# Kernel optimization log

Measured on AMD Instinct MI355X. Metric: run time of the kernel, lower is better.

## Reference

```python
import jax, jax.numpy as jnp
import numpy as np

H = 128

def setup_inputs() -> dict:
    key = jax.random.key(0)
    ks = jax.random.split(key, 7)
    x = jax.random.normal(ks[0], (4, 65536, H), dtype=jnp.float32)
    # Linear(3H -> H) and Linear(H -> H), torch-style fan-in init scale
    W1 = jax.random.normal(ks[1], (3 * H, H), dtype=jnp.float32) / np.sqrt(3 * H)
    b1 = jax.random.normal(ks[2], (H,), dtype=jnp.float32) * 0.01
    W2 = jax.random.normal(ks[3], (H, H), dtype=jnp.float32) / np.sqrt(H)
    b2 = jax.random.normal(ks[4], (H,), dtype=jnp.float32) * 0.01
    gamma = jnp.ones((H,), dtype=jnp.float32)
    beta = jnp.zeros((H,), dtype=jnp.float32)
    return {"x": x, "W1": W1, "b1": b1, "W2": W2, "b2": b2, "gamma": gamma, "beta": beta}


def _layernorm(h, gamma, beta, eps=1e-5):
    mu = jnp.mean(h, axis=-1, keepdims=True)
    var = jnp.var(h, axis=-1, keepdims=True)
    return (h - mu) * jax.lax.rsqrt(var + eps) * gamma + beta


def reference(x, W1, b1, W2, b2, gamma, beta):
    # circular neighbor gather along node dim
    prev_x = jnp.roll(x, 1, axis=1)
    next_x = jnp.roll(x, -1, axis=1)
    cat = jnp.concatenate([prev_x, x, next_x], axis=-1)  # [B, N, 3H]
    h = jax.nn.relu(jnp.einsum('bnc,ch->bnh', cat, W1) + b1)
    delta = jnp.einsum('bnh,hk->bnk', h, W2) + b2
    return jax.nn.relu(_layernorm(x + delta, gamma, beta))
```

## Files before the change

### kernel.cpp

```cpp
#include <hip/hip_runtime.h>


typedef __bf16 bf16x8 __attribute__((ext_vector_type(8)));
typedef __bf16 bf16x4 __attribute__((ext_vector_type(4)));
typedef float  f32x4  __attribute__((ext_vector_type(4)));

#define H      128
#define NB     65536
#define TILE   64
#define XS     136
#define HSS    136
#define PSS    18
#define NTILES 4096
#define GRID   512

__global__ __launch_bounds__(256, 2)
void cbb_kernel(const float* __restrict__ x, const float* __restrict__ W1,
                const float* __restrict__ b1, const float* __restrict__ W2,
                const float* __restrict__ b2, const float* __restrict__ gamma,
                const float* __restrict__ beta, float* __restrict__ out) {
    __shared__ __align__(16) char raw[(66 * XS + 64 * HSS) * 2];
    __bf16* xs = (__bf16*)raw;
    __bf16* hs = xs + 66 * XS;
    __shared__ __align__(16) __bf16 w2s[16384];
    __shared__ __align__(16) float2 ps2[64 * PSS];

    const int tid  = threadIdx.x;
    const int wid  = tid >> 6;
    const int lane = tid & 63;
    const int l    = lane & 15;
    const int g    = lane >> 4;
    const int col0 = wid * 32;

    const f32x4 b1v[2] = { *(const f32x4*)(b1 + col0 + g * 4),
                           *(const f32x4*)(b1 + col0 + 16 + g * 4) };
    const f32x4 b2v[2] = { *(const f32x4*)(b2 + col0 + g * 4),
                           *(const f32x4*)(b2 + col0 + 16 + g * 4) };
    const f32x4 gmv[2] = { *(const f32x4*)(gamma + col0 + g * 4),
                           *(const f32x4*)(gamma + col0 + 16 + g * 4) };
    const f32x4 btv[2] = { *(const f32x4*)(beta + col0 + g * 4),
                           *(const f32x4*)(beta + col0 + 16 + g * 4) };

    bf16x8 w1f[12][2];
#pragma unroll
    for (int ks = 0; ks < 12; ++ks) {
#pragma unroll
        for (int ct = 0; ct < 2; ++ct) {
            const int cc = col0 + ct * 16 + l;
            bf16x8 f;
#pragma unroll
            for (int j = 0; j < 8; ++j)
                f[j] = (__bf16)W1[(ks * 32 + g * 8 + j) * H + cc];
            w1f[ks][ct] = f;
        }
    }

    for (int idx = tid; idx < 16384; idx += 256) {
        const int j  = idx & 7;
        const int ln = (idx >> 3) & 63;
        const int ct = (idx >> 9) & 1;
        const int ks = (idx >> 10) & 3;
        const int w  = idx >> 12;
        const int row = ks * 32 + (ln >> 4) * 8 + j;
        const int col = w * 32 + ct * 16 + (ln & 15);
        w2s[idx] = (__bf16)W2[row * H + col];
    }
    const __bf16* w2w = w2s + wid * 4096;

    float4 xreg[8];
    float4 xhalo;
    {
        const int t  = blockIdx.x;
        const int b  = t >> 10;
        const int n0 = (t & 1023) << 6;
        const size_t rowbase = (size_t)b * NB;
#pragma unroll
        for (int s = 0; s < 8; ++s) {
            const int q = tid + s * 256;
            const int r = q >> 5, c = q & 31;
            const int grow = (n0 - 1 + r + NB) & (NB - 1);
            xreg[s] = *(const float4*)(x + ((rowbase + grow) * H + c * 4));
        }
        if (tid < 64) {
            const int q = 2048 + tid;
            const int r = q >> 5, c = q & 31;
            const int grow = (n0 - 1 + r + NB) & (NB - 1);
            xhalo = *(const float4*)(x + ((rowbase + grow) * H + c * 4));
        }
    }

    for (int t = blockIdx.x; t < NTILES; t += GRID) {
        const int b  = t >> 10;
        const int n0 = (t & 1023) << 6;
        const size_t rowbase = (size_t)b * NB;

        __syncthreads();

#pragma unroll
        for (int s = 0; s < 8; ++s) {
            const int q = tid + s * 256;
            const int r = q >> 5, c = q & 31;
            bf16x4 v4;
            v4[0] = (__bf16)xreg[s].x; v4[1] = (__bf16)xreg[s].y;
            v4[2] = (__bf16)xreg[s].z; v4[3] = (__bf16)xreg[s].w;
            *(bf16x4*)(xs + r * XS + c * 4) = v4;
        }
        if (tid < 64) {
            const int q = 2048 + tid;
            const int r = q >> 5, c = q & 31;
            bf16x4 v4;
            v4[0] = (__bf16)xhalo.x; v4[1] = (__bf16)xhalo.y;
            v4[2] = (__bf16)xhalo.z; v4[3] = (__bf16)xhalo.w;
            *(bf16x4*)(xs + r * XS + c * 4) = v4;
        }
        __syncthreads();

        if (t + GRID < NTILES) {
            const int tn  = t + GRID;
            const int bn  = tn >> 10;
            const int n0n = (tn & 1023) << 6;
            const size_t rbn = (size_t)bn * NB;
#pragma unroll
            for (int s = 0; s < 8; ++s) {
                const int q = tid + s * 256;
                const int r = q >> 5, c = q & 31;
                const int grow = (n0n - 1 + r + NB) & (NB - 1);
                xreg[s] = *(const float4*)(x + ((rbn + grow) * H + c * 4));
            }
            if (tid < 64) {
                const int q = 2048 + tid;
                const int r = q >> 5, c = q & 31;
                const int grow = (n0n - 1 + r + NB) & (NB - 1);
                xhalo = *(const float4*)(x + ((rbn + grow) * H + c * 4));
            }
        }

        f32x4 acc[4][2];
#pragma unroll
        for (int rt = 0; rt < 4; ++rt)
#pragma unroll
            for (int ct = 0; ct < 2; ++ct)
                acc[rt][ct] = (f32x4){0.f, 0.f, 0.f, 0.f};

        __builtin_amdgcn_s_setprio(1);
#pragma unroll
        for (int ks = 0; ks < 12; ++ks) {
            const int k  = ks * 32 + g * 8;
            const int ro = k >> 7, kc = k & 127;
#pragma unroll
            for (int rt = 0; rt < 4; ++rt) {
                const bf16x8 a = *(const bf16x8*)(xs + (rt * 16 + l + ro) * XS + kc);
                acc[rt][0] = __builtin_amdgcn_mfma_f32_16x16x32_bf16(w1f[ks][0], a, acc[rt][0], 0, 0, 0);
                acc[rt][1] = __builtin_amdgcn_mfma_f32_16x16x32_bf16(w1f[ks][1], a, acc[rt][1], 0, 0, 0);
            }
        }
        __builtin_amdgcn_s_setprio(0);

#pragma unroll
        for (int rt = 0; rt < 4; ++rt) {
#pragma unroll
            for (int ct = 0; ct < 2; ++ct) {
                bf16x4 hv;
#pragma unroll
                for (int i = 0; i < 4; ++i)
                    hv[i] = (__bf16)fmaxf(acc[rt][ct][i] + b1v[ct][i], 0.f);
                *(bf16x4*)(hs + (rt * 16 + l) * HSS + col0 + ct * 16 + g * 4) = hv;
            }
        }
        __syncthreads();

        f32x4 acc2[4][2];
#pragma unroll
        for (int rt = 0; rt < 4; ++rt)
#pragma unroll
            for (int ct = 0; ct < 2; ++ct)
                acc2[rt][ct] = (f32x4){0.f, 0.f, 0.f, 0.f};

        __builtin_amdgcn_s_setprio(1);
#pragma unroll
        for (int ks = 0; ks < 4; ++ks) {
            const bf16x8 wf0 = *(const bf16x8*)(w2w + ks * 1024 + lane * 8);
            const bf16x8 wf1 = *(const bf16x8*)(w2w + ks * 1024 + 512 + lane * 8);
#pragma unroll
            for (int rt = 0; rt < 4; ++rt) {
                const bf16x8 a = *(const bf16x8*)(hs + (rt * 16 + l) * HSS + ks * 32 + g * 8);
                acc2[rt][0] = __builtin_amdgcn_mfma_f32_16x16x32_bf16(wf0, a, acc2[rt][0], 0, 0, 0);
                acc2[rt][1] = __builtin_amdgcn_mfma_f32_16x16x32_bf16(wf1, a, acc2[rt][1], 0, 0, 0);
            }
        }
        __builtin_amdgcn_s_setprio(0);

#pragma unroll
        for (int rt = 0; rt < 4; ++rt) {
#pragma unroll
            for (int ct = 0; ct < 2; ++ct) {
                const bf16x4 xv = *(const bf16x4*)(xs + (rt * 16 + l + 1) * XS + col0 + ct * 16 + g * 4);
#pragma unroll
                for (int i = 0; i < 4; ++i)
                    acc2[rt][ct][i] += b2v[ct][i] + (float)xv[i];
            }
        }

#pragma unroll
        for (int rt = 0; rt < 4; ++rt) {
            float s = 0.f, qq = 0.f;
#pragma unroll
            for (int ct = 0; ct < 2; ++ct)
#pragma unroll
                for (int i = 0; i < 4; ++i) {
                    const float v = acc2[rt][ct][i];
                    s += v; qq += v * v;
                }
            ps2[(rt * 16 + l) * PSS + wid * 4 + g] = make_float2(s, qq);
        }
        __syncthreads();

        float mu, rv;
        {
            const int ar = g * 16 + l;
            const f32x4* pp = (const f32x4*)(ps2 + ar * PSS);
            float S = 0.f, Q = 0.f;
#pragma unroll
            for (int j = 0; j < 8; ++j) {
                const f32x4 e = pp[j];
                S += e[0] + e[2];
                Q += e[1] + e[3];
            }
            mu = S * (1.f / 128.f);
            const float var = Q * (1.f / 128.f) - mu * mu;
            rv = rsqrtf(var + 1e-5f);
        }

#pragma unroll
        for (int rt = 0; rt < 4; ++rt) {
            const float mur = __shfl(mu, (lane & 15) + rt * 16);
            const float rvr = __shfl(rv, (lane & 15) + rt * 16);
            float* op = out + (rowbase + n0 + rt * 16 + l) * H + col0;
#pragma unroll
            for (int ct = 0; ct < 2; ++ct) {
                f32x4 o;
#pragma unroll
                for (int i = 0; i < 4; ++i)
                    o[i] = fmaxf((acc2[rt][ct][i] - mur) * rvr * gmv[ct][i] + btv[ct][i], 0.f);
                *(f32x4*)(op + ct * 16 + g * 4) = o;
            }
        }
    }
}

extern "C" void kernel_launch(void* const* d_in, const int* in_sizes, int n_in,
                              void* d_out, int out_size, void* d_ws, size_t ws_size,
                              hipStream_t stream) {
    const float* x     = (const float*)d_in[0];
    const float* W1    = (const float*)d_in[1];
    const float* b1    = (const float*)d_in[2];
    const float* W2    = (const float*)d_in[3];
    const float* b2    = (const float*)d_in[4];
    const float* gamma = (const float*)d_in[5];
    const float* beta  = (const float*)d_in[6];
    float* out = (float*)d_out;

    cbb_kernel<<<GRID, 256, 0, stream>>>(x, W1, b1, W2, b2, gamma, beta, out);
}
```

Measured before the change: 321.7 us.

## Double block size to 8 waves, each owning 16 output columns

Raises the block to 512 threads, so each of 8 waves computes 16 output columns instead of 32. This halves the per-wave W1 register fragments and accumulators, and the x staging per thread. Bias, gamma and beta now live in shared memory, and LayerNorm partial sums are reduced across lanes with xor shuffles before one lane writes them. The now-redundant barrier at the loop head is dropped. The goal is more resident waves per CU to hide memory latency. The cost is more work per block in the staging, shuffle and reduction steps, plus a tighter register budget from launch_bounds(512,4) that could cause spills.

```diff
diff --git a/kernel.cpp b/kernel.cpp
--- a/kernel.cpp
+++ b/kernel.cpp
@@ -13,8 +13,9 @@
 #define PSS    18
 #define NTILES 4096
 #define GRID   512
-
-__global__ __launch_bounds__(256, 2)
+#define BLK    512
+
+__global__ __launch_bounds__(BLK, 4)
 void cbb_kernel(const float* __restrict__ x, const float* __restrict__ W1,
                 const float* __restrict__ b1, const float* __restrict__ W2,
                 const float* __restrict__ b2, const float* __restrict__ gamma,
@@ -24,50 +25,42 @@
     __bf16* hs = xs + 66 * XS;
     __shared__ __align__(16) __bf16 w2s[16384];
     __shared__ __align__(16) float2 ps2[64 * PSS];
+    __shared__ __align__(16) float s_b1[128], s_b2[128], s_gamma[128], s_beta[128];
 
     const int tid  = threadIdx.x;
     const int wid  = tid >> 6;
     const int lane = tid & 63;
     const int l    = lane & 15;
     const int g    = lane >> 4;
-    const int col0 = wid * 32;
-
-    const f32x4 b1v[2] = { *(const f32x4*)(b1 + col0 + g * 4),
-                           *(const f32x4*)(b1 + col0 + 16 + g * 4) };
-    const f32x4 b2v[2] = { *(const f32x4*)(b2 + col0 + g * 4),
-                           *(const f32x4*)(b2 + col0 + 16 + g * 4) };
-    const f32x4 gmv[2] = { *(const f32x4*)(gamma + col0 + g * 4),
-                           *(const f32x4*)(gamma + col0 + 16 + g * 4) };
-    const f32x4 btv[2] = { *(const f32x4*)(beta + col0 + g * 4),
-                           *(const f32x4*)(beta + col0 + 16 + g * 4) };
-
-    bf16x8 w1f[12][2];
+    const int col0 = wid * 16;
+
+    if (tid < 128) {
+        s_b1[tid] = b1[tid];   s_b2[tid]   = b2[tid];
+        s_gamma[tid] = gamma[tid]; s_beta[tid] = beta[tid];
+    }
+
+    bf16x8 w1f[12];
 #pragma unroll
     for (int ks = 0; ks < 12; ++ks) {
-#pragma unroll
-        for (int ct = 0; ct < 2; ++ct) {
-            const int cc = col0 + ct * 16 + l;
-            bf16x8 f;
-#pragma unroll
-            for (int j = 0; j < 8; ++j)
-                f[j] = (__bf16)W1[(ks * 32 + g * 8 + j) * H + cc];
-            w1f[ks][ct] = f;
-        }
-    }
-
-    for (int idx = tid; idx < 16384; idx += 256) {
+        bf16x8 f;
+#pragma unroll
+        for (int j = 0; j < 8; ++j)
+            f[j] = (__bf16)W1[(ks * 32 + g * 8 + j) * H + col0 + l];
+        w1f[ks] = f;
+    }
+
+    for (int idx = tid; idx < 16384; idx += BLK) {
         const int j  = idx & 7;
         const int ln = (idx >> 3) & 63;
-        const int ct = (idx >> 9) & 1;
-        const int ks = (idx >> 10) & 3;
-        const int w  = idx >> 12;
+        const int ks = (idx >> 9) & 3;
+        const int w  = idx >> 11;
         const int row = ks * 32 + (ln >> 4) * 8 + j;
-        const int col = w * 32 + ct * 16 + (ln & 15);
+        const int col = w * 16 + (ln & 15);
         w2s[idx] = (__bf16)W2[row * H + col];
     }
-    const __bf16* w2w = w2s + wid * 4096;
-
-    float4 xreg[8];
+    const __bf16* w2w = w2s + wid * 2048;
+
+    float4 xreg[4];
     float4 xhalo;
     {
         const int t  = blockIdx.x;
@@ -75,8 +68,8 @@
         const int n0 = (t & 1023) << 6;
         const size_t rowbase = (size_t)b * NB;
 #pragma unroll
-        for (int s = 0; s < 8; ++s) {
-            const int q = tid + s * 256;
+        for (int s = 0; s < 4; ++s) {
+            const int q = tid + s * BLK;
             const int r = q >> 5, c = q & 31;
             const int grow = (n0 - 1 + r + NB) & (NB - 1);
             xreg[s] = *(const float4*)(x + ((rowbase + grow) * H + c * 4));
@@ -94,11 +87,10 @@
         const int n0 = (t & 1023) << 6;
         const size_t rowbase = (size_t)b * NB;
 
-        __syncthreads();
-
-#pragma unroll
-        for (int s = 0; s < 8; ++s) {
-            const int q = tid + s * 256;
+
+#pragma unroll
+        for (int s = 0; s < 4; ++s) {
+            const int q = tid + s * BLK;
             const int r = q >> 5, c = q & 31;
             bf16x4 v4;
             v4[0] = (__bf16)xreg[s].x; v4[1] = (__bf16)xreg[s].y;
@@ -121,8 +113,8 @@
             const int n0n = (tn & 1023) << 6;
             const size_t rbn = (size_t)bn * NB;
 #pragma unroll
-            for (int s = 0; s < 8; ++s) {
-                const int q = tid + s * 256;
+            for (int s = 0; s < 4; ++s) {
+                const int q = tid + s * BLK;
                 const int r = q >> 5, c = q & 31;
                 const int grow = (n0n - 1 + r + NB) & (NB - 1);
                 xreg[s] = *(const float4*)(x + ((rbn + grow) * H + c * 4));
@@ -135,12 +127,10 @@
             }
         }
 
-        f32x4 acc[4][2];
+        f32x4 acc[4];
 #pragma unroll
         for (int rt = 0; rt < 4; ++rt)
-#pragma unroll
-            for (int ct = 0; ct < 2; ++ct)
-                acc[rt][ct] = (f32x4){0.f, 0.f, 0.f, 0.f};
+            acc[rt] = (f32x4){0.f, 0.f, 0.f, 0.f};
 
         __builtin_amdgcn_s_setprio(1);
 #pragma unroll
@@ -150,54 +140,49 @@
 #pragma unroll
             for (int rt = 0; rt < 4; ++rt) {
                 const bf16x8 a = *(const bf16x8*)(xs + (rt * 16 + l + ro) * XS + kc);
-                acc[rt][0] = __builtin_amdgcn_mfma_f32_16x16x32_bf16(w1f[ks][0], a, acc[rt][0], 0, 0, 0);
-                acc[rt][1] = __builtin_amdgcn_mfma_f32_16x16x32_bf16(w1f[ks][1], a, acc[rt][1], 0, 0, 0);
+                acc[rt] = __builtin_amdgcn_mfma_f32_16x16x32_bf16(w1f[ks], a, acc[rt], 0, 0, 0);
             }
         }
         __builtin_amdgcn_s_setprio(0);
 
-#pragma unroll
-        for (int rt = 0; rt < 4; ++rt) {
-#pragma unroll
-            for (int ct = 0; ct < 2; ++ct) {
+        {
+            const f32x4 b1q = *(const f32x4*)(s_b1 + col0 + g * 4);
+#pragma unroll
+            for (int rt = 0; rt < 4; ++rt) {
                 bf16x4 hv;
 #pragma unroll
                 for (int i = 0; i < 4; ++i)
-                    hv[i] = (__bf16)fmaxf(acc[rt][ct][i] + b1v[ct][i], 0.f);
-                *(bf16x4*)(hs + (rt * 16 + l) * HSS + col0 + ct * 16 + g * 4) = hv;
+                    hv[i] = (__bf16)fmaxf(acc[rt][i] + b1q[i], 0.f);
+                *(bf16x4*)(hs + (rt * 16 + l) * HSS + col0 + g * 4) = hv;
             }
         }
         __syncthreads();
 
-        f32x4 acc2[4][2];
+        f32x4 acc2[4];
 #pragma unroll
         for (int rt = 0; rt < 4; ++rt)
-#pragma unroll
-            for (int ct = 0; ct < 2; ++ct)
-                acc2[rt][ct] = (f32x4){0.f, 0.f, 0.f, 0.f};
+            acc2[rt] = (f32x4){0.f, 0.f, 0.f, 0.f};
 
         __builtin_amdgcn_s_setprio(1);
 #pragma unroll
         for (int ks = 0; ks < 4; ++ks) {
-            const bf16x8 wf0 = *(const bf16x8*)(w2w + ks * 1024 + lane * 8);
-            const bf16x8 wf1 = *(const bf16x8*)(w2w + ks * 1024 + 512 + lane * 8);
+            const bf16x8 wf = *(const bf16x8*)(w2w + ks * 512 + lane * 8);
 #pragma unroll
             for (int rt = 0; rt < 4; ++rt) {
                 const bf16x8 a = *(const bf16x8*)(hs + (rt * 16 + l) * HSS + ks * 32 + g * 8);
-                acc2[rt][0] = __builtin_amdgcn_mfma_f32_16x16x32_bf16(wf0, a, acc2[rt][0], 0, 0, 0);
-                acc2[rt][1] = __builtin_amdgcn_mfma_f32_16x16x32_bf16(wf1, a, acc2[rt][1], 0, 0, 0);
+                acc2[rt] = __builtin_amdgcn_mfma_f32_16x16x32_bf16(wf, a, acc2[rt], 0, 0, 0);
             }
         }
         __builtin_amdgcn_s_setprio(0);
 
-#pragma unroll
-        for (int rt = 0; rt < 4; ++rt) {
-#pragma unroll
-            for (int ct = 0; ct < 2; ++ct) {
-                const bf16x4 xv = *(const bf16x4*)(xs + (rt * 16 + l + 1) * XS + col0 + ct * 16 + g * 4);
+        {
+            const f32x4 b2q = *(const f32x4*)(s_b2 + col0 + g * 4);
+#pragma unroll
+            for (int rt = 0; rt < 4; ++rt) {
+                const bf16x4 xv = *(const bf16x4*)(xs + (rt * 16 + l + 1) * XS + col0 + g * 4);
 #pragma unroll
                 for (int i = 0; i < 4; ++i)
-                    acc2[rt][ct][i] += b2v[ct][i] + (float)xv[i];
+                    acc2[rt][i] += b2q[i] + (float)xv[i];
             }
         }
 
@@ -205,23 +190,23 @@
         for (int rt = 0; rt < 4; ++rt) {
             float s = 0.f, qq = 0.f;
 #pragma unroll
-            for (int ct = 0; ct < 2; ++ct)
-#pragma unroll
-                for (int i = 0; i < 4; ++i) {
-                    const float v = acc2[rt][ct][i];
-                    s += v; qq += v * v;
-                }
-            ps2[(rt * 16 + l) * PSS + wid * 4 + g] = make_float2(s, qq);
+            for (int i = 0; i < 4; ++i) {
+                const float v = acc2[rt][i];
+                s += v; qq += v * v;
+            }
+            s  += __shfl_xor(s, 16);  s  += __shfl_xor(s, 32);
+            qq += __shfl_xor(qq, 16); qq += __shfl_xor(qq, 32);
+            if (g == 0)
+                ps2[(rt * 16 + l) * PSS + wid] = make_float2(s, qq);
         }
         __syncthreads();
 
         float mu, rv;
         {
-            const int ar = g * 16 + l;
-            const f32x4* pp = (const f32x4*)(ps2 + ar * PSS);
+            const f32x4* pp = (const f32x4*)(ps2 + lane * PSS);
             float S = 0.f, Q = 0.f;
 #pragma unroll
-            for (int j = 0; j < 8; ++j) {
+            for (int j = 0; j < 4; ++j) {
                 const f32x4 e = pp[j];
                 S += e[0] + e[2];
                 Q += e[1] + e[3];
@@ -231,18 +216,19 @@
             rv = rsqrtf(var + 1e-5f);
         }
 
-#pragma unroll
-        for (int rt = 0; rt < 4; ++rt) {
-            const float mur = __shfl(mu, (lane & 15) + rt * 16);
-            const float rvr = __shfl(rv, (lane & 15) + rt * 16);
-            float* op = out + (rowbase + n0 + rt * 16 + l) * H + col0;
-#pragma unroll
-            for (int ct = 0; ct < 2; ++ct) {
+        {
+            const f32x4 gm = *(const f32x4*)(s_gamma + col0 + g * 4);
+            const f32x4 bt = *(const f32x4*)(s_beta + col0 + g * 4);
+#pragma unroll
+            for (int rt = 0; rt < 4; ++rt) {
+                const float mur = __shfl(mu, (lane & 15) + rt * 16);
+                const float rvr = __shfl(rv, (lane & 15) + rt * 16);
+                float* op = out + (rowbase + n0 + rt * 16 + l) * H + col0;
                 f32x4 o;
 #pragma unroll
                 for (int i = 0; i < 4; ++i)
-                    o[i] = fmaxf((acc2[rt][ct][i] - mur) * rvr * gmv[ct][i] + btv[ct][i], 0.f);
-                *(f32x4*)(op + ct * 16 + g * 4) = o;
+                    o[i] = fmaxf((acc2[rt][i] - mur) * rvr * gm[i] + bt[i], 0.f);
+                *(f32x4*)(op + g * 4) = o;
             }
         }
     }
@@ -260,5 +246,5 @@
     const float* beta  = (const float*)d_in[6];
     float* out = (float*)d_out;
 
-    cbb_kernel<<<GRID, 256, 0, stream>>>(x, W1, b1, W2, b2, gamma, beta, out);
+    cbb_kernel<<<GRID, BLK, 0, stream>>>(x, W1, b1, W2, b2, gamma, beta, out);
 }
```

After: 268.6 us. -16.5%, faster.
